# Optimization experiments

Hardware: AMD Instinct MI355X
Metric: run time of the kernel (lower is better)

Reference implementation:

```python
import jax, jax.numpy as jnp
import numpy as np

H, NH, NKV, HD, FF = 2048, 16, 8, 128, 6144
S, T = 2048, 4096
EPS, THETA, NEG = 1e-6, 1e6, -1e9

def _rms(x, w, eps=EPS):
    return x * jax.lax.rsqrt(jnp.mean(x * x, axis=-1, keepdims=True) + eps) * w

def _rotate_half(x):
    d = x.shape[-1] // 2
    return jnp.concatenate([-x[..., d:], x[..., :d]], axis=-1)

def _rope(positions, hd, theta=THETA):
    inv_freq = 1.0 / (theta ** (jnp.arange(0, hd, 2, dtype=jnp.float32) / hd))
    freqs = positions.astype(jnp.float32)[..., None] * inv_freq  # [B,S,hd/2]
    emb = jnp.concatenate([freqs, freqs], axis=-1)               # [B,S,hd]
    return jnp.cos(emb), jnp.sin(emb)

def setup_inputs() -> dict:
    key = jax.random.key(0)
    ks = jax.random.split(key, 12)
    hidden_states = jax.random.normal(ks[0], (1, S, H), jnp.float32) * 0.02
    i = jnp.arange(T)
    causal_mask = jnp.where(i[None, :] <= i[:, None], 0.0, NEG).astype(jnp.float32)[None, None]
    idxs = jnp.sort(jax.random.randint(ks[1], (S,), 0, T - 1, jnp.int32)).at[-1].set(T - 1)
    w = lambda k, sh: jax.random.normal(k, sh, jnp.float32) * 0.02
    return dict(
        hidden_states=hidden_states, causal_mask=causal_mask,
        keys_idxs=idxs, hs_idxs=idxs, positions=idxs[None, :],
        ln_in_w=jnp.ones((H,), jnp.float32),
        q_w=w(ks[2], (H, NH * HD)), k_w=w(ks[3], (H, NKV * HD)), v_w=w(ks[4], (H, NKV * HD)),
        q_norm_w=jnp.ones((HD,), jnp.float32), k_norm_w=jnp.ones((HD,), jnp.float32),
        o_w=w(ks[5], (NH * HD, H)), ln_post_w=jnp.ones((H,), jnp.float32),
        gate_w=w(ks[6], (H, FF)), up_w=w(ks[7], (H, FF)), down_w=w(ks[8], (FF, H)),
    )

def reference(hidden_states, causal_mask, keys_idxs, hs_idxs, positions,
              ln_in_w, q_w, k_w, v_w, q_norm_w, k_norm_w, o_w,
              ln_post_w, gate_w, up_w, down_w):
    B, Sq, _ = hidden_states.shape
    hd = q_norm_w.shape[0]
    nh = q_w.shape[1] // hd
    nkv = k_w.shape[1] // hd
    scaling = hd ** -0.5

    # gather pruned causal mask: index_select dim 3 (keys), then dim 2 (queries)
    mask = causal_mask[:, :, :, keys_idxs][:, :, hs_idxs, :]  # [B,1,Sq,Sk]

    cos, sin = _rope(positions, hd)  # [B,Sq,hd]

    x = _rms(hidden_states, ln_in_w)
    q = _rms((x @ q_w).reshape(B, Sq, nh, hd), q_norm_w).swapaxes(1, 2)   # [B,nh,Sq,hd]
    k = _rms((x @ k_w).reshape(B, Sq, nkv, hd), k_norm_w).swapaxes(1, 2)  # [B,nkv,Sq,hd]
    v = (x @ v_w).reshape(B, Sq, nkv, hd).swapaxes(1, 2)

    c, s = cos[:, None], sin[:, None]
    q = q * c + _rotate_half(q) * s
    k = k * c + _rotate_half(k) * s

    groups = nh // nkv
    k_rep = jnp.repeat(k, groups, axis=1)
    v_rep = jnp.repeat(v, groups, axis=1)

    # token-importance from last query (last original token kept at slot Sq-1)
    q_last = q[:, :, -1:, :]
    imp = jax.nn.softmax(jnp.einsum('bhqd,bhkd->bhqk', q_last, k_rep) * scaling, axis=-1)
    importance = imp[0, :, 0, :].mean(axis=0)
    importance = jax.lax.stop_gradient(importance.at[Sq - 1].set(jnp.inf))

    scores = jnp.einsum('bhqd,bhkd->bhqk', q, k_rep) * scaling + mask
    attn = jax.nn.softmax(scores, axis=-1)
    ctx = jnp.einsum('bhqk,bhkd->bhqd', attn, v_rep)
    attn_out = ctx.swapaxes(1, 2).reshape(B, Sq, nh * hd) @ o_w

    h = hidden_states + attn_out
    y = _rms(h, ln_post_w)
    mlp = (jax.nn.silu(y @ gate_w) * (y @ up_w)) @ down_w
    out = h + mlp
    return out, importance
```

## Files before the change

kernel.cpp:

```cpp
#include <hip/hip_runtime.h>
#include <math.h>

#define S_LEN 2048
#define HDIM  2048
#define NHEADS 16
#define NKVH   8
#define HD     128
#define FFDIM  6144
#define EPSV   1e-6f

__device__ __forceinline__ ushort f2bf(float f) {
    unsigned u = __float_as_uint(f);
    u += 0x7FFF + ((u >> 16) & 1);
    return (ushort)(u >> 16);
}
__device__ __forceinline__ float bf2f(ushort h) {
    return __uint_as_float(((unsigned)h) << 16);
}

typedef __attribute__((ext_vector_type(8))) short bf16x8;
typedef __attribute__((ext_vector_type(4))) float f32x4;

__device__ __forceinline__ void glds16(const void* g, void* l) {
    __builtin_amdgcn_global_load_lds(
        (const __attribute__((address_space(1))) void*)g,
        (__attribute__((address_space(3))) void*)l, 16, 0, 0);
}

__global__ __launch_bounds__(256) void rmsnorm_split_k(const float* __restrict__ in,
                                                       const float* __restrict__ w,
                                                       ushort* __restrict__ oh,
                                                       ushort* __restrict__ ol) {
    int s = blockIdx.x;
    int tid = threadIdx.x;
    const float* row = in + (size_t)s * HDIM;
    float ss = 0.0f;
    for (int i = tid; i < HDIM; i += 256) {
        float v = row[i];
        ss += v * v;
    }
    __shared__ float red[256];
    red[tid] = ss;
    __syncthreads();
    for (int off = 128; off > 0; off >>= 1) {
        if (tid < off) red[tid] += red[tid + off];
        __syncthreads();
    }
    float r = rsqrtf(red[0] / (float)HDIM + EPSV);
    for (int i = tid; i < HDIM; i += 256) {
        float v = row[i] * r * w[i];
        ushort h = f2bf(v);
        oh[(size_t)s * HDIM + i] = h;
        ol[(size_t)s * HDIM + i] = f2bf(v - bf2f(h));
    }
}

__global__ __launch_bounds__(256) void split_k(const float* __restrict__ in,
                                               ushort* __restrict__ oh,
                                               ushort* __restrict__ ol, int n) {
    int i = blockIdx.x * 256 + threadIdx.x;
    if (i < n) {
        float v = in[i];
        ushort h = f2bf(v);
        oh[i] = h;
        ol[i] = f2bf(v - bf2f(h));
    }
}

__global__ __launch_bounds__(256) void conv_k_swz_k(const float* __restrict__ in,
                                                    ushort* __restrict__ oh,
                                                    ushort* __restrict__ ol) {
    int i = blockIdx.x * 256 + threadIdx.x;
    int s = i >> 10;
    int d = i & 127;
    int base = i & ~127;
    float v = in[i];
    unsigned u = __float_as_uint(v);
    float hi = __uint_as_float(u & 0xFFFF0000u);
    int o = base + (d ^ ((s & 7) << 3));
    oh[o] = (ushort)(u >> 16);
    ol[o] = (ushort)(__float_as_uint(v - hi) >> 16);
}

__global__ __launch_bounds__(256) void conv_vt_k(const float* __restrict__ v,
                                                 ushort* __restrict__ oh,
                                                 ushort* __restrict__ ol) {
    __shared__ float t[64][65];
    int s0 = blockIdx.x * 64, d0 = blockIdx.y * 64, kvh = blockIdx.z;
    int tid = threadIdx.x;
#pragma unroll
    for (int p = 0; p < 4; ++p) {
        int c = tid + p * 256;
        int ss = c >> 4, d4 = (c & 15) * 4;
        float4 x = *(const float4*)&v[((size_t)(s0 + ss) * NKVH + kvh) * HD + d0 + d4];
        t[d4 + 0][ss] = x.x;
        t[d4 + 1][ss] = x.y;
        t[d4 + 2][ss] = x.z;
        t[d4 + 3][ss] = x.w;
    }
    __syncthreads();
#pragma unroll
    for (int p = 0; p < 4; ++p) {
        int c = tid + p * 256;
        int dd = c >> 4, s4 = (c & 15) * 4;
        int d = d0 + dd;
        int sx = s4 ^ ((d & 7) << 3);
        size_t obase = ((size_t)kvh * HD + d) * S_LEN + s0 + sx;
        ushort4 hv, lv;
        float a0 = t[dd][s4 + 0], a1 = t[dd][s4 + 1], a2 = t[dd][s4 + 2], a3 = t[dd][s4 + 3];
        unsigned u0 = __float_as_uint(a0), u1 = __float_as_uint(a1);
        unsigned u2 = __float_as_uint(a2), u3 = __float_as_uint(a3);
        hv.x = (ushort)(u0 >> 16); lv.x = (ushort)(__float_as_uint(a0 - __uint_as_float(u0 & 0xFFFF0000u)) >> 16);
        hv.y = (ushort)(u1 >> 16); lv.y = (ushort)(__float_as_uint(a1 - __uint_as_float(u1 & 0xFFFF0000u)) >> 16);
        hv.z = (ushort)(u2 >> 16); lv.z = (ushort)(__float_as_uint(a2 - __uint_as_float(u2 & 0xFFFF0000u)) >> 16);
        hv.w = (ushort)(u3 >> 16); lv.w = (ushort)(__float_as_uint(a3 - __uint_as_float(u3 & 0xFFFF0000u)) >> 16);
        *(ushort4*)&oh[obase] = hv;
        *(ushort4*)&ol[obase] = lv;
    }
}

__global__ __launch_bounds__(256) void transpose_split_k(const float* __restrict__ W,
                                                         ushort* __restrict__ Th,
                                                         ushort* __restrict__ Tl,
                                                         int K, int Ntot, int n0) {
    __shared__ float t[64][65];
    int tid = threadIdx.x;
    int nt = blockIdx.x * 64;
    int kt = blockIdx.y * 64;
#pragma unroll
    for (int p = 0; p < 4; ++p) {
        int idx = tid + p * 256;
        int kk = idx >> 4;
        int nn = (idx & 15) * 4;
        float4 v = *(const float4*)&W[(size_t)(kt + kk) * Ntot + n0 + nt + nn];
        t[nn + 0][kk] = v.x;
        t[nn + 1][kk] = v.y;
        t[nn + 2][kk] = v.z;
        t[nn + 3][kk] = v.w;
    }
    __syncthreads();
#pragma unroll
    for (int p = 0; p < 4; ++p) {
        int idx = tid + p * 256;
        int nn = idx >> 4;
        int kk = (idx & 15) * 4;
        ushort4 hv, lv;
        float a0 = t[nn][kk + 0], a1 = t[nn][kk + 1], a2 = t[nn][kk + 2], a3 = t[nn][kk + 3];
        hv.x = f2bf(a0); lv.x = f2bf(a0 - bf2f(hv.x));
        hv.y = f2bf(a1); lv.y = f2bf(a1 - bf2f(hv.y));
        hv.z = f2bf(a2); lv.z = f2bf(a2 - bf2f(hv.z));
        hv.w = f2bf(a3); lv.w = f2bf(a3 - bf2f(hv.w));
        size_t o = (size_t)(nt + nn) * K + kt + kk;
        *(ushort4*)&Th[o] = hv;
        *(ushort4*)&Tl[o] = lv;
    }
}

template <int MODE>
__global__ __launch_bounds__(256, 3) void gemm_bf16x3(
    const ushort* __restrict__ Ah, const ushort* __restrict__ Al,
    const ushort* __restrict__ Bh, const ushort* __restrict__ Bl,
    const float* res, const float* __restrict__ gbuf,
    float* C, ushort* __restrict__ Dh, ushort* __restrict__ Dl,
    int M, int N, int K) {
    __shared__ __align__(16) ushort sAh[128 * 32];
    __shared__ __align__(16) ushort sAl[128 * 32];
    __shared__ __align__(16) ushort sBh[128 * 32];
    __shared__ __align__(16) ushort sBl[128 * 32];

    unsigned nbx = gridDim.x;
    unsigned flat = blockIdx.y * nbx + blockIdx.x;
    unsigned cpx = (nbx * gridDim.y) >> 3;
    unsigned sflat = (flat & 7u) * cpx + (flat >> 3);
    int bx = (int)(sflat % nbx);
    int by = (int)(sflat / nbx);
    int bm = by * 128, bn = bx * 128;

    int tid = threadIdx.x;
    int lane = tid & 63, wave = tid >> 6;
    int wr = wave >> 1, wc = wave & 1;
    int r = lane & 15, kq = lane >> 4;

    int srow = tid >> 2;
    int sk = (tid & 3) * 8;
    const ushort* gA0h = Ah + (size_t)(bm + srow) * K + sk;
    const ushort* gA0l = Al + (size_t)(bm + srow) * K + sk;
    const ushort* gB0h = Bh + (size_t)(bn + srow) * K + sk;
    const ushort* gB0l = Bl + (size_t)(bn + srow) * K + sk;
    const size_t rstep = (size_t)64 * K;

    const ushort* pAh = sAh + (wr * 64 + r) * 32 + kq * 8;
    const ushort* pAl = sAl + (wr * 64 + r) * 32 + kq * 8;
    const ushort* pBh = sBh + (wc * 64 + r) * 32 + kq * 8;
    const ushort* pBl = sBl + (wc * 64 + r) * 32 + kq * 8;

    f32x4 acc[4][4] = {};

    for (int k0 = 0; k0 < K; k0 += 32) {
        glds16(gA0h, sAh + tid * 8);
        glds16(gA0h + rstep, sAh + 2048 + tid * 8);
        glds16(gA0l, sAl + tid * 8);
        glds16(gA0l + rstep, sAl + 2048 + tid * 8);
        glds16(gB0h, sBh + tid * 8);
        glds16(gB0h + rstep, sBh + 2048 + tid * 8);
        glds16(gB0l, sBl + tid * 8);
        glds16(gB0l + rstep, sBl + 2048 + tid * 8);
        gA0h += 32; gA0l += 32; gB0h += 32; gB0l += 32;
        __syncthreads();

        bf16x8 ah[4], al[4];
#pragma unroll
        for (int mi = 0; mi < 4; ++mi) {
            ah[mi] = *(const bf16x8*)(pAh + mi * 512);
            al[mi] = *(const bf16x8*)(pAl + mi * 512);
        }
#pragma unroll
        for (int ni = 0; ni < 4; ++ni) {
            bf16x8 bh = *(const bf16x8*)(pBh + ni * 512);
            bf16x8 bl = *(const bf16x8*)(pBl + ni * 512);
#pragma unroll
            for (int mi = 0; mi < 4; ++mi) {
                acc[mi][ni] = __builtin_amdgcn_mfma_f32_16x16x32_bf16(ah[mi], bh, acc[mi][ni], 0, 0, 0);
                acc[mi][ni] = __builtin_amdgcn_mfma_f32_16x16x32_bf16(al[mi], bh, acc[mi][ni], 0, 0, 0);
                acc[mi][ni] = __builtin_amdgcn_mfma_f32_16x16x32_bf16(ah[mi], bl, acc[mi][ni], 0, 0, 0);
            }
        }
        __syncthreads();
    }

    int c0 = bn + wc * 64 + r;
    int r0 = bm + wr * 64 + kq * 4;
#pragma unroll
    for (int mi = 0; mi < 4; ++mi)
#pragma unroll
        for (int ni = 0; ni < 4; ++ni)
#pragma unroll
            for (int j = 0; j < 4; ++j) {
                int row = r0 + mi * 16 + j;
                int col = c0 + ni * 16;
                size_t idx = (size_t)row * N + col;
                float val = acc[mi][ni][j];
                if (MODE == 0) {
                    if (res) val += res[idx];
                    C[idx] = val;
                } else {
                    float gv = gbuf[idx];
                    float dv = gv / (1.0f + expf(-gv)) * val;
                    ushort hh = f2bf(dv);
                    Dh[idx] = hh;
                    Dl[idx] = f2bf(dv - bf2f(hh));
                }
            }
}

__global__ __launch_bounds__(128) void qk_norm_rope_k(float* __restrict__ qk,
                                                      const float* __restrict__ nw,
                                                      const int* __restrict__ positions,
                                                      int nheads) {
    int s = blockIdx.x;
    int h = blockIdx.y;
    int d = threadIdx.x;
    float* row = qk + ((size_t)s * nheads + h) * HD;
    __shared__ float buf[HD];
    __shared__ float red[HD];
    float v = row[d];
    red[d] = v * v;
    __syncthreads();
    for (int off = 64; off > 0; off >>= 1) {
        if (d < off) red[d] += red[d + off];
        __syncthreads();
    }
    float r = rsqrtf(red[0] / (float)HD + EPSV);
    float nv = v * r * nw[d];
    buf[d] = nv;
    __syncthreads();
    float pos = (float)positions[s];
    int d2 = d & 63;
    float inv_freq = expf(-((float)(2 * d2) / 128.0f) * 13.815510557964274f);
    float freq = pos * inv_freq;
    float c, sn;
    sincosf(freq, &sn, &c);
    float rot = (d < 64) ? -buf[d + 64] : buf[d - 64];
    row[d] = nv * c + rot * sn;
}

#define ATQ 64
#define ATK 64

__global__ __launch_bounds__(256, 2) void attn_mfma_k(
    const ushort* __restrict__ Qhg, const ushort* __restrict__ Qlg,
    const ushort* __restrict__ Khg, const ushort* __restrict__ Klg,
    const ushort* __restrict__ Vhg, const ushort* __restrict__ Vlg,
    const int* __restrict__ keys_idxs, const int* __restrict__ hs_idxs,
    ushort* __restrict__ Chg, ushort* __restrict__ Clg) {
    __shared__ __align__(16) ushort sKh[64 * 128];
    __shared__ __align__(16) ushort sKl[64 * 128];
    __shared__ __align__(16) ushort sVh[128 * 64];
    __shared__ __align__(16) ushort sVl[128 * 64];
    __shared__ int kidx[ATK];
    __shared__ int qpos[ATQ];

    int bx = blockIdx.x;
    int qt = (bx & 1) ? (31 - (bx >> 1)) : (bx >> 1);
    int h = blockIdx.y;
    int kvh = h >> 1;
    int tid = threadIdx.x;
    int lane = tid & 63, wv = tid >> 6;
    int q0 = qt * ATQ;
    int r = lane & 15, kq = lane >> 4;
    int xorv = (lane & 7) << 3;
    const float scale = 0.088388347648318447f;

    bf16x8 qh[4], ql[4];
    {
        const ushort* qb = Qhg + ((size_t)(q0 + wv * 16 + r) * NHEADS + h) * HD + kq * 8;
        const ushort* qb2 = Qlg + ((size_t)(q0 + wv * 16 + r) * NHEADS + h) * HD + kq * 8;
#pragma unroll
        for (int ks = 0; ks < 4; ++ks) {
            qh[ks] = *(const bf16x8*)(qb + ks * 32);
            ql[ks] = *(const bf16x8*)(qb2 + ks * 32);
        }
    }
    if (tid < ATQ) qpos[tid] = hs_idxs[q0 + tid];

    const size_t kvstride = (size_t)NKVH * HD;
    const ushort* gKh = Khg + ((size_t)(tid >> 4) * NKVH + kvh) * HD + (tid & 15) * 8;
    const ushort* gKl = Klg + ((size_t)(tid >> 4) * NKVH + kvh) * HD + (tid & 15) * 8;
    const ushort* gVh = Vhg + ((size_t)kvh * HD + (tid >> 3)) * S_LEN + (tid & 7) * 8;
    const ushort* gVl = Vlg + ((size_t)kvh * HD + (tid >> 3)) * S_LEN + (tid & 7) * 8;

    f32x4 o[8] = {};
    float m_run[4] = {-3.0e38f, -3.0e38f, -3.0e38f, -3.0e38f};
    float l_run[4] = {0.0f, 0.0f, 0.0f, 0.0f};

    __syncthreads();
    int hs_max = qpos[ATQ - 1];
    int qp[4];
#pragma unroll
    for (int j = 0; j < 4; ++j) qp[j] = qpos[wv * 16 + kq * 4 + j];

    for (int kt = 0; kt < S_LEN / ATK; ++kt) {
        int k0 = kt * ATK;
        if (keys_idxs[k0] > hs_max) break;
        __syncthreads();
        const size_t koff = (size_t)k0 * kvstride;
#pragma unroll
        for (int p = 0; p < 4; ++p) {
            glds16(gKh + koff + (size_t)p * 16 * kvstride, sKh + (tid + p * 256) * 8);
            glds16(gKl + koff + (size_t)p * 16 * kvstride, sKl + (tid + p * 256) * 8);
            glds16(gVh + k0 + (size_t)p * 32 * S_LEN, sVh + (tid + p * 256) * 8);
            glds16(gVl + k0 + (size_t)p * 32 * S_LEN, sVl + (tid + p * 256) * 8);
        }
        if (tid < ATK) kidx[tid] = keys_idxs[k0 + tid];
        __syncthreads();

        f32x4 sf[4] = {};
#pragma unroll
        for (int ks = 0; ks < 4; ++ks) {
            int kb = (ks * 32 + kq * 8) ^ xorv;
#pragma unroll
            for (int f = 0; f < 4; ++f) {
                bf16x8 kh = *(const bf16x8*)(sKh + (f * 16 + r) * 128 + kb);
                bf16x8 kl = *(const bf16x8*)(sKl + (f * 16 + r) * 128 + kb);
                sf[f] = __builtin_amdgcn_mfma_f32_16x16x32_bf16(qh[ks], kh, sf[f], 0, 0, 0);
                sf[f] = __builtin_amdgcn_mfma_f32_16x16x32_bf16(ql[ks], kh, sf[f], 0, 0, 0);
                sf[f] = __builtin_amdgcn_mfma_f32_16x16x32_bf16(qh[ks], kl, sf[f], 0, 0, 0);
            }
        }

        int kj[4];
#pragma unroll
        for (int f = 0; f < 4; ++f) kj[f] = kidx[f * 16 + r];
        float alj[4];
#pragma unroll
        for (int j = 0; j < 4; ++j) {
#pragma unroll
            for (int f = 0; f < 4; ++f)
                sf[f][j] = sf[f][j] * scale + ((kj[f] <= qp[j]) ? 0.0f : -1.0e9f);
            float m0 = fmaxf(fmaxf(sf[0][j], sf[1][j]), fmaxf(sf[2][j], sf[3][j]));
#pragma unroll
            for (int off = 1; off < 16; off <<= 1) m0 = fmaxf(m0, __shfl_xor(m0, off));
            float mn = fmaxf(m_run[j], m0);
            alj[j] = __expf(m_run[j] - mn);
            m_run[j] = mn;
            float rsum = 0.0f;
#pragma unroll
            for (int f = 0; f < 4; ++f) {
                sf[f][j] = __expf(sf[f][j] - mn);
                rsum += sf[f][j];
            }
#pragma unroll
            for (int off = 1; off < 16; off <<= 1) rsum += __shfl_xor(rsum, off);
            l_run[j] = l_run[j] * alj[j] + rsum;
        }
#pragma unroll
        for (int df = 0; df < 8; ++df)
#pragma unroll
            for (int j = 0; j < 4; ++j) o[df][j] *= alj[j];

        __syncthreads();

        ushort* sPh = sKh + wv * 2048;
        ushort* sPl = sPh + 1024;
#pragma unroll
        for (int j = 0; j < 4; ++j) {
            int qloc = kq * 4 + j;
            int swz = (qloc & 7) << 3;
            int rowb = qloc * 64;
#pragma unroll
            for (int f = 0; f < 4; ++f) {
                float pv = sf[f][j];
                unsigned u = __float_as_uint(pv);
                float hi = __uint_as_float(u & 0xFFFF0000u);
                int a = rowb + ((f * 16 + r) ^ swz);
                sPh[a] = (ushort)(u >> 16);
                sPl[a] = (ushort)(__float_as_uint(pv - hi) >> 16);
            }
        }

#pragma unroll
        for (int kv0 = 0; kv0 < 2; ++kv0) {
            int kb = (kv0 * 32 + kq * 8) ^ xorv;
            bf16x8 pah = *(const bf16x8*)(sPh + r * 64 + kb);
            bf16x8 pal = *(const bf16x8*)(sPl + r * 64 + kb);
#pragma unroll
            for (int df = 0; df < 8; ++df) {
                bf16x8 vh = *(const bf16x8*)(sVh + (df * 16 + r) * 64 + kb);
                bf16x8 vl = *(const bf16x8*)(sVl + (df * 16 + r) * 64 + kb);
                o[df] = __builtin_amdgcn_mfma_f32_16x16x32_bf16(pah, vh, o[df], 0, 0, 0);
                o[df] = __builtin_amdgcn_mfma_f32_16x16x32_bf16(pal, vh, o[df], 0, 0, 0);
                o[df] = __builtin_amdgcn_mfma_f32_16x16x32_bf16(pah, vl, o[df], 0, 0, 0);
            }
        }
    }

#pragma unroll
    for (int j = 0; j < 4; ++j) {
        float invl = 1.0f / l_run[j];
        int qg = q0 + wv * 16 + kq * 4 + j;
#pragma unroll
        for (int df = 0; df < 8; ++df) {
            int d = df * 16 + r;
            float val = o[df][j] * invl;
            size_t idx = ((size_t)qg * NHEADS + h) * HD + d;
            ushort hh = f2bf(val);
            Chg[idx] = hh;
            Clg[idx] = f2bf(val - bf2f(hh));
        }
    }
}

__global__ __launch_bounds__(256) void importance_scores_k(const float* __restrict__ q,
                                                           const float* __restrict__ k,
                                                           float* __restrict__ imp_ws) {
    int h = blockIdx.x;
    int kv = h >> 1;
    int tid = threadIdx.x;
    __shared__ float qrow[HD];
    __shared__ float sc[S_LEN];
    __shared__ float red[256];
    const float* qp = q + ((size_t)(S_LEN - 1) * NHEADS + h) * HD;
    if (tid < HD) qrow[tid] = qp[tid];
    __syncthreads();
    const float scale = 0.088388347648318447f;
    float lmax = -3.0e38f;
#pragma unroll
    for (int rep = 0; rep < 8; ++rep) {
        int j = tid + rep * 256;
        const float* kp = k + ((size_t)j * NKVH + kv) * HD;
        float dot = 0.0f;
        for (int d = 0; d < HD; ++d) dot += qrow[d] * kp[d];
        float sval = dot * scale;
        sc[j] = sval;
        lmax = fmaxf(lmax, sval);
    }
    red[tid] = lmax;
    __syncthreads();
    for (int off = 128; off > 0; off >>= 1) {
        if (tid < off) red[tid] = fmaxf(red[tid], red[tid + off]);
        __syncthreads();
    }
    float m = red[0];
    __syncthreads();
    float lsum = 0.0f;
    float evals[8];
#pragma unroll
    for (int rep = 0; rep < 8; ++rep) {
        int j = tid + rep * 256;
        float e = expf(sc[j] - m);
        evals[rep] = e;
        lsum += e;
    }
    red[tid] = lsum;
    __syncthreads();
    for (int off = 128; off > 0; off >>= 1) {
        if (tid < off) red[tid] += red[tid + off];
        __syncthreads();
    }
    float inv = 1.0f / red[0];
#pragma unroll
    for (int rep = 0; rep < 8; ++rep) {
        int j = tid + rep * 256;
        imp_ws[(size_t)h * S_LEN + j] = evals[rep] * inv;
    }
}

__global__ __launch_bounds__(256) void importance_combine_k(const float* __restrict__ imp_ws,
                                                            float* __restrict__ out) {
    int j = blockIdx.x * 256 + threadIdx.x;
    float sum = 0.0f;
    for (int h = 0; h < NHEADS; ++h) sum += imp_ws[(size_t)h * S_LEN + j];
    out[j] = (j == S_LEN - 1) ? 3.0e38f : sum * (1.0f / NHEADS);
}

extern "C" void kernel_launch(void* const* d_in, const int* in_sizes, int n_in,
                              void* d_out, int out_size, void* d_ws, size_t ws_size,
                              hipStream_t stream) {
    const float* hidden    = (const float*)d_in[0];
    const int*   keys_idxs = (const int*)d_in[2];
    const int*   hs_idxs   = (const int*)d_in[3];
    const int*   positions = (const int*)d_in[4];
    const float* ln_in_w   = (const float*)d_in[5];
    const float* q_w       = (const float*)d_in[6];
    const float* k_w       = (const float*)d_in[7];
    const float* v_w       = (const float*)d_in[8];
    const float* q_norm_w  = (const float*)d_in[9];
    const float* k_norm_w  = (const float*)d_in[10];
    const float* o_w       = (const float*)d_in[11];
    const float* ln_post_w = (const float*)d_in[12];
    const float* gate_w    = (const float*)d_in[13];
    const float* up_w      = (const float*)d_in[14];
    const float* down_w    = (const float*)d_in[15];

    float* out = (float*)d_out;
    float* ws = (float*)d_ws;
    const size_t MF = 1024ull * 1024;

    ushort* Xh = (ushort*)(ws);
    ushort* Xl = (ushort*)(ws + 2 * MF);
    ushort* Wh = (ushort*)(ws + 4 * MF);
    ushort* Wl = (ushort*)(ws + 6 * MF);
    float*  qb  = ws + 8 * MF;
    float*  kbf = ws + 12 * MF;
    float*  vbf = ws + 14 * MF;
    ushort* Qbh = (ushort*)(ws);
    ushort* Qbl = (ushort*)(ws + 2 * MF);
    float*  imp = ws + 4 * MF;
    ushort* Kbh = (ushort*)(ws + 4 * MF);
    ushort* Kbl = (ushort*)(ws + 5 * MF);
    ushort* Vth = (ushort*)(ws + 6 * MF);
    ushort* Vtl = (ushort*)(ws + 7 * MF);
    ushort* Ch = (ushort*)(ws + 8 * MF);
    ushort* Cl = (ushort*)(ws + 10 * MF);
    float*  hb = ws + 12 * MF;
    ushort* Yh = (ushort*)(ws + 16 * MF);
    ushort* Yl = (ushort*)(ws + 18 * MF);
    float*  gb = ws + 8 * MF;
    ushort* Dh = (ushort*)(ws + 12 * MF);
    ushort* Dl = (ushort*)(ws + 14 * MF);

    rmsnorm_split_k<<<S_LEN, 256, 0, stream>>>(hidden, ln_in_w, Xh, Xl);

    transpose_split_k<<<dim3(32, 32), 256, 0, stream>>>(q_w, Wh, Wl, HDIM, HDIM, 0);
    gemm_bf16x3<0><<<dim3(HDIM / 128, S_LEN / 128), 256, 0, stream>>>(
        Xh, Xl, Wh, Wl, nullptr, nullptr, qb, nullptr, nullptr, S_LEN, HDIM, HDIM);

    transpose_split_k<<<dim3(16, 32), 256, 0, stream>>>(k_w, Wh, Wl, HDIM, 1024, 0);
    gemm_bf16x3<0><<<dim3(1024 / 128, S_LEN / 128), 256, 0, stream>>>(
        Xh, Xl, Wh, Wl, nullptr, nullptr, kbf, nullptr, nullptr, S_LEN, 1024, HDIM);

    transpose_split_k<<<dim3(16, 32), 256, 0, stream>>>(v_w, Wh, Wl, HDIM, 1024, 0);
    gemm_bf16x3<0><<<dim3(1024 / 128, S_LEN / 128), 256, 0, stream>>>(
        Xh, Xl, Wh, Wl, nullptr, nullptr, vbf, nullptr, nullptr, S_LEN, 1024, HDIM);

    qk_norm_rope_k<<<dim3(S_LEN, NHEADS), 128, 0, stream>>>(qb, q_norm_w, positions, NHEADS);
    qk_norm_rope_k<<<dim3(S_LEN, NKVH), 128, 0, stream>>>(kbf, k_norm_w, positions, NKVH);

    importance_scores_k<<<NHEADS, 256, 0, stream>>>(qb, kbf, imp);
    importance_combine_k<<<S_LEN / 256, 256, 0, stream>>>(imp, out + (size_t)S_LEN * HDIM);

    split_k<<<(S_LEN * NHEADS * HD) / 256, 256, 0, stream>>>(qb, Qbh, Qbl, S_LEN * NHEADS * HD);
    conv_k_swz_k<<<(S_LEN * NKVH * HD) / 256, 256, 0, stream>>>(kbf, Kbh, Kbl);
    conv_vt_k<<<dim3(S_LEN / 64, HD / 64, NKVH), 256, 0, stream>>>(vbf, Vth, Vtl);

    attn_mfma_k<<<dim3(S_LEN / ATQ, NHEADS), 256, 0, stream>>>(
        Qbh, Qbl, Kbh, Kbl, Vth, Vtl, keys_idxs, hs_idxs, Ch, Cl);

    transpose_split_k<<<dim3(32, 32), 256, 0, stream>>>(o_w, Wh, Wl, HDIM, HDIM, 0);
    gemm_bf16x3<0><<<dim3(HDIM / 128, S_LEN / 128), 256, 0, stream>>>(
        Ch, Cl, Wh, Wl, hidden, nullptr, hb, nullptr, nullptr, S_LEN, HDIM, HDIM);

    hipMemcpyAsync(out, hb, (size_t)S_LEN * HDIM * sizeof(float),
                   hipMemcpyDeviceToDevice, stream);

    rmsnorm_split_k<<<S_LEN, 256, 0, stream>>>(hb, ln_post_w, Yh, Yl);

    for (int c = 0; c < 3; ++c) {
        transpose_split_k<<<dim3(32, 32), 256, 0, stream>>>(gate_w, Wh, Wl, HDIM, FFDIM, c * 2048);
        gemm_bf16x3<0><<<dim3(16, 16), 256, 0, stream>>>(
            Yh, Yl, Wh, Wl, nullptr, nullptr, gb, nullptr, nullptr, S_LEN, 2048, HDIM);
        transpose_split_k<<<dim3(32, 32), 256, 0, stream>>>(up_w, Wh, Wl, HDIM, FFDIM, c * 2048);
        gemm_bf16x3<1><<<dim3(16, 16), 256, 0, stream>>>(
            Yh, Yl, Wh, Wl, nullptr, gb, nullptr, Dh, Dl, S_LEN, 2048, HDIM);
        transpose_split_k<<<dim3(32, 32), 256, 0, stream>>>(
            down_w + (size_t)c * 2048 * HDIM, Wh, Wl, 2048, HDIM, 0);
        gemm_bf16x3<0><<<dim3(16, 16), 256, 0, stream>>>(
            Dh, Dl, Wh, Wl, out, nullptr, out, nullptr, nullptr, S_LEN, HDIM, 2048);
    }
}
```

Baseline: 1.687 ms.

## Double-buffer GEMM LDS staging and merge QKV and gate/up GEMMs

The GEMM kernel now double-buffers its LDS tiles, so the global-to-LDS load of the next K slice is issued before the MFMA work on the current one, and one barrier per iteration is removed. Occupancy drops to 2 blocks per CU because LDS use doubles. The Q/K/V projections are merged into one wide GEMM writing a strided qkv buffer, and gate/up are merged into one N=4096 GEMM. SiLU*mul moves into a separate elementwise kernel, which adds an extra round trip through global memory but gives larger launches and reuses the A tiles.

```diff
diff --git a/kernel.cpp b/kernel.cpp
--- a/kernel.cpp
+++ b/kernel.cpp
@@ -55,34 +55,32 @@
     }
 }
 
-__global__ __launch_bounds__(256) void split_k(const float* __restrict__ in,
-                                               ushort* __restrict__ oh,
-                                               ushort* __restrict__ ol, int n) {
+__global__ __launch_bounds__(256) void conv_q_k(const float* __restrict__ in,
+                                                ushort* __restrict__ oh,
+                                                ushort* __restrict__ ol) {
     int i = blockIdx.x * 256 + threadIdx.x;
-    if (i < n) {
-        float v = in[i];
-        ushort h = f2bf(v);
-        oh[i] = h;
-        ol[i] = f2bf(v - bf2f(h));
-    }
+    int s = i >> 11, c = i & 2047;
+    float v = in[(size_t)s * 4096 + c];
+    ushort h = f2bf(v);
+    oh[i] = h;
+    ol[i] = f2bf(v - bf2f(h));
 }
 
 __global__ __launch_bounds__(256) void conv_k_swz_k(const float* __restrict__ in,
                                                     ushort* __restrict__ oh,
                                                     ushort* __restrict__ ol) {
     int i = blockIdx.x * 256 + threadIdx.x;
-    int s = i >> 10;
-    int d = i & 127;
-    int base = i & ~127;
-    float v = in[i];
+    int s = i >> 10, c = i & 1023;
+    int d = c & 127;
+    float v = in[(size_t)s * 4096 + 2048 + c];
     unsigned u = __float_as_uint(v);
     float hi = __uint_as_float(u & 0xFFFF0000u);
-    int o = base + (d ^ ((s & 7) << 3));
+    int o = (i & ~127) + (d ^ ((s & 7) << 3));
     oh[o] = (ushort)(u >> 16);
     ol[o] = (ushort)(__float_as_uint(v - hi) >> 16);
 }
 
-__global__ __launch_bounds__(256) void conv_vt_k(const float* __restrict__ v,
+__global__ __launch_bounds__(256) void conv_vt_k(const float* __restrict__ vsrc,
                                                  ushort* __restrict__ oh,
                                                  ushort* __restrict__ ol) {
     __shared__ float t[64][65];
@@ -92,7 +90,7 @@
     for (int p = 0; p < 4; ++p) {
         int c = tid + p * 256;
         int ss = c >> 4, d4 = (c & 15) * 4;
-        float4 x = *(const float4*)&v[((size_t)(s0 + ss) * NKVH + kvh) * HD + d0 + d4];
+        float4 x = *(const float4*)&vsrc[(size_t)(s0 + ss) * 4096 + 3072 + kvh * 128 + d0 + d4];
         t[d4 + 0][ss] = x.x;
         t[d4 + 1][ss] = x.y;
         t[d4 + 2][ss] = x.z;
@@ -122,7 +120,8 @@
 __global__ __launch_bounds__(256) void transpose_split_k(const float* __restrict__ W,
                                                          ushort* __restrict__ Th,
                                                          ushort* __restrict__ Tl,
-                                                         int K, int Ntot, int n0) {
+                                                         int K, int Ntot, int n0,
+                                                         int nout0) {
     __shared__ float t[64][65];
     int tid = threadIdx.x;
     int nt = blockIdx.x * 64;
@@ -150,23 +149,21 @@
         hv.y = f2bf(a1); lv.y = f2bf(a1 - bf2f(hv.y));
         hv.z = f2bf(a2); lv.z = f2bf(a2 - bf2f(hv.z));
         hv.w = f2bf(a3); lv.w = f2bf(a3 - bf2f(hv.w));
-        size_t o = (size_t)(nt + nn) * K + kt + kk;
+        size_t o = (size_t)(nout0 + nt + nn) * K + kt + kk;
         *(ushort4*)&Th[o] = hv;
         *(ushort4*)&Tl[o] = lv;
     }
 }
 
-template <int MODE>
-__global__ __launch_bounds__(256, 3) void gemm_bf16x3(
+__global__ __launch_bounds__(256, 2) void gemm_bf16x3(
     const ushort* __restrict__ Ah, const ushort* __restrict__ Al,
     const ushort* __restrict__ Bh, const ushort* __restrict__ Bl,
-    const float* res, const float* __restrict__ gbuf,
-    float* C, ushort* __restrict__ Dh, ushort* __restrict__ Dl,
+    const float* __restrict__ res, float* __restrict__ C,
     int M, int N, int K) {
-    __shared__ __align__(16) ushort sAh[128 * 32];
-    __shared__ __align__(16) ushort sAl[128 * 32];
-    __shared__ __align__(16) ushort sBh[128 * 32];
-    __shared__ __align__(16) ushort sBl[128 * 32];
+    __shared__ __align__(16) ushort sAh[2][128 * 32];
+    __shared__ __align__(16) ushort sAl[2][128 * 32];
+    __shared__ __align__(16) ushort sBh[2][128 * 32];
+    __shared__ __align__(16) ushort sBl[2][128 * 32];
 
     unsigned nbx = gridDim.x;
     unsigned flat = blockIdx.y * nbx + blockIdx.x;
@@ -183,31 +180,29 @@
 
     int srow = tid >> 2;
     int sk = (tid & 3) * 8;
-    const ushort* gA0h = Ah + (size_t)(bm + srow) * K + sk;
-    const ushort* gA0l = Al + (size_t)(bm + srow) * K + sk;
-    const ushort* gB0h = Bh + (size_t)(bn + srow) * K + sk;
-    const ushort* gB0l = Bl + (size_t)(bn + srow) * K + sk;
+    const ushort* gAh = Ah + (size_t)(bm + srow) * K + sk;
+    const ushort* gAl = Al + (size_t)(bm + srow) * K + sk;
+    const ushort* gBh = Bh + (size_t)(bn + srow) * K + sk;
+    const ushort* gBl = Bl + (size_t)(bn + srow) * K + sk;
     const size_t rstep = (size_t)64 * K;
 
-    const ushort* pAh = sAh + (wr * 64 + r) * 32 + kq * 8;
-    const ushort* pAl = sAl + (wr * 64 + r) * 32 + kq * 8;
-    const ushort* pBh = sBh + (wc * 64 + r) * 32 + kq * 8;
-    const ushort* pBl = sBl + (wc * 64 + r) * 32 + kq * 8;
-
     f32x4 acc[4][4] = {};
 
-    for (int k0 = 0; k0 < K; k0 += 32) {
-        glds16(gA0h, sAh + tid * 8);
-        glds16(gA0h + rstep, sAh + 2048 + tid * 8);
-        glds16(gA0l, sAl + tid * 8);
-        glds16(gA0l + rstep, sAl + 2048 + tid * 8);
-        glds16(gB0h, sBh + tid * 8);
-        glds16(gB0h + rstep, sBh + 2048 + tid * 8);
-        glds16(gB0l, sBl + tid * 8);
-        glds16(gB0l + rstep, sBl + 2048 + tid * 8);
-        gA0h += 32; gA0l += 32; gB0h += 32; gB0l += 32;
-        __syncthreads();
-
+    auto STAGE = [&](int buf, int k0) {
+        glds16(gAh + k0, &sAh[buf][tid * 8]);
+        glds16(gAh + k0 + rstep, &sAh[buf][2048 + tid * 8]);
+        glds16(gAl + k0, &sAl[buf][tid * 8]);
+        glds16(gAl + k0 + rstep, &sAl[buf][2048 + tid * 8]);
+        glds16(gBh + k0, &sBh[buf][tid * 8]);
+        glds16(gBh + k0 + rstep, &sBh[buf][2048 + tid * 8]);
+        glds16(gBl + k0, &sBl[buf][tid * 8]);
+        glds16(gBl + k0 + rstep, &sBl[buf][2048 + tid * 8]);
+    };
+    auto COMPUTE = [&](int buf) {
+        const ushort* pAh = &sAh[buf][(wr * 64 + r) * 32 + kq * 8];
+        const ushort* pAl = &sAl[buf][(wr * 64 + r) * 32 + kq * 8];
+        const ushort* pBh = &sBh[buf][(wc * 64 + r) * 32 + kq * 8];
+        const ushort* pBl = &sBl[buf][(wc * 64 + r) * 32 + kq * 8];
         bf16x8 ah[4], al[4];
 #pragma unroll
         for (int mi = 0; mi < 4; ++mi) {
@@ -225,8 +220,18 @@
                 acc[mi][ni] = __builtin_amdgcn_mfma_f32_16x16x32_bf16(ah[mi], bl, acc[mi][ni], 0, 0, 0);
             }
         }
-        __syncthreads();
-    }
+    };
+
+    STAGE(0, 0);
+    __syncthreads();
+    int cur = 0;
+    for (int k0 = 32; k0 < K; k0 += 32) {
+        STAGE(cur ^ 1, k0);
+        COMPUTE(cur);
+        __syncthreads();
+        cur ^= 1;
+    }
+    COMPUTE(cur);
 
     int c0 = bn + wc * 64 + r;
     int r0 = bm + wr * 64 + kq * 4;
@@ -240,27 +245,19 @@
                 int col = c0 + ni * 16;
                 size_t idx = (size_t)row * N + col;
                 float val = acc[mi][ni][j];
-                if (MODE == 0) {
-                    if (res) val += res[idx];
-                    C[idx] = val;
-                } else {
-                    float gv = gbuf[idx];
-                    float dv = gv / (1.0f + expf(-gv)) * val;
-                    ushort hh = f2bf(dv);
-                    Dh[idx] = hh;
-                    Dl[idx] = f2bf(dv - bf2f(hh));
-                }
+                if (res) val += res[idx];
+                C[idx] = val;
             }
 }
 
 __global__ __launch_bounds__(128) void qk_norm_rope_k(float* __restrict__ qk,
                                                       const float* __restrict__ nw,
                                                       const int* __restrict__ positions,
-                                                      int nheads) {
+                                                      int stride) {
     int s = blockIdx.x;
     int h = blockIdx.y;
     int d = threadIdx.x;
-    float* row = qk + ((size_t)s * nheads + h) * HD;
+    float* row = qk + (size_t)s * stride + (size_t)h * HD;
     __shared__ float buf[HD];
     __shared__ float red[HD];
     float v = row[d];
@@ -452,14 +449,15 @@
 
 __global__ __launch_bounds__(256) void importance_scores_k(const float* __restrict__ q,
                                                            const float* __restrict__ k,
-                                                           float* __restrict__ imp_ws) {
+                                                           float* __restrict__ imp_ws,
+                                                           int stride) {
     int h = blockIdx.x;
     int kv = h >> 1;
     int tid = threadIdx.x;
     __shared__ float qrow[HD];
     __shared__ float sc[S_LEN];
     __shared__ float red[256];
-    const float* qp = q + ((size_t)(S_LEN - 1) * NHEADS + h) * HD;
+    const float* qp = q + (size_t)(S_LEN - 1) * stride + (size_t)h * HD;
     if (tid < HD) qrow[tid] = qp[tid];
     __syncthreads();
     const float scale = 0.088388347648318447f;
@@ -467,7 +465,7 @@
 #pragma unroll
     for (int rep = 0; rep < 8; ++rep) {
         int j = tid + rep * 256;
-        const float* kp = k + ((size_t)j * NKVH + kv) * HD;
+        const float* kp = k + (size_t)j * stride + (size_t)kv * HD;
         float dot = 0.0f;
         for (int d = 0; d < HD; ++d) dot += qrow[d] * kp[d];
         float sval = dot * scale;
@@ -511,6 +509,19 @@
     float sum = 0.0f;
     for (int h = 0; h < NHEADS; ++h) sum += imp_ws[(size_t)h * S_LEN + j];
     out[j] = (j == S_LEN - 1) ? 3.0e38f : sum * (1.0f / NHEADS);
+}
+
+__global__ __launch_bounds__(256) void silu_split_k(const float* __restrict__ gu,
+                                                    ushort* __restrict__ dh,
+                                                    ushort* __restrict__ dl) {
+    int i = blockIdx.x * 256 + threadIdx.x;
+    int s = i >> 11, c = i & 2047;
+    const float* row = gu + (size_t)s * 4096;
+    float g = row[c], u = row[c + 2048];
+    float d = g / (1.0f + expf(-g)) * u;
+    ushort hh = f2bf(d);
+    dh[i] = hh;
+    dl[i] = f2bf(d - bf2f(hh));
 }
 
 extern "C" void kernel_launch(void* const* d_in, const int* in_sizes, int n_in,
@@ -536,59 +547,55 @@
     float* ws = (float*)d_ws;
     const size_t MF = 1024ull * 1024;
 
-    ushort* Xh = (ushort*)(ws);
-    ushort* Xl = (ushort*)(ws + 2 * MF);
-    ushort* Wh = (ushort*)(ws + 4 * MF);
-    ushort* Wl = (ushort*)(ws + 6 * MF);
-    float*  qb  = ws + 8 * MF;
-    float*  kbf = ws + 12 * MF;
-    float*  vbf = ws + 14 * MF;
+    ushort* Xh  = (ushort*)(ws);
+    ushort* Xl  = (ushort*)(ws + 2 * MF);
+    ushort* Wh  = (ushort*)(ws + 4 * MF);
+    ushort* Wl  = (ushort*)(ws + 8 * MF);
+    float*  qkv = ws + 12 * MF;
     ushort* Qbh = (ushort*)(ws);
     ushort* Qbl = (ushort*)(ws + 2 * MF);
-    float*  imp = ws + 4 * MF;
     ushort* Kbh = (ushort*)(ws + 4 * MF);
     ushort* Kbl = (ushort*)(ws + 5 * MF);
     ushort* Vth = (ushort*)(ws + 6 * MF);
     ushort* Vtl = (ushort*)(ws + 7 * MF);
-    ushort* Ch = (ushort*)(ws + 8 * MF);
-    ushort* Cl = (ushort*)(ws + 10 * MF);
-    float*  hb = ws + 12 * MF;
-    ushort* Yh = (ushort*)(ws + 16 * MF);
-    ushort* Yl = (ushort*)(ws + 18 * MF);
-    float*  gb = ws + 8 * MF;
-    ushort* Dh = (ushort*)(ws + 12 * MF);
-    ushort* Dl = (ushort*)(ws + 14 * MF);
+    float*  imp = ws + 8 * MF;
+    ushort* Woh = (ushort*)(ws + 4 * MF);
+    ushort* Wol = (ushort*)(ws + 6 * MF);
+    ushort* Ch  = (ushort*)(ws + 12 * MF);
+    ushort* Cl  = (ushort*)(ws + 14 * MF);
+    float*  hb  = ws + 16 * MF;
+    ushort* Yh  = (ushort*)(ws);
+    ushort* Yl  = (ushort*)(ws + 2 * MF);
+    float*  gu  = ws + 12 * MF;
+    ushort* Dh  = (ushort*)(ws + 4 * MF);
+    ushort* Dl  = (ushort*)(ws + 6 * MF);
+    ushort* Wdh = (ushort*)(ws + 8 * MF);
+    ushort* Wdl = (ushort*)(ws + 10 * MF);
 
     rmsnorm_split_k<<<S_LEN, 256, 0, stream>>>(hidden, ln_in_w, Xh, Xl);
 
-    transpose_split_k<<<dim3(32, 32), 256, 0, stream>>>(q_w, Wh, Wl, HDIM, HDIM, 0);
-    gemm_bf16x3<0><<<dim3(HDIM / 128, S_LEN / 128), 256, 0, stream>>>(
-        Xh, Xl, Wh, Wl, nullptr, nullptr, qb, nullptr, nullptr, S_LEN, HDIM, HDIM);
-
-    transpose_split_k<<<dim3(16, 32), 256, 0, stream>>>(k_w, Wh, Wl, HDIM, 1024, 0);
-    gemm_bf16x3<0><<<dim3(1024 / 128, S_LEN / 128), 256, 0, stream>>>(
-        Xh, Xl, Wh, Wl, nullptr, nullptr, kbf, nullptr, nullptr, S_LEN, 1024, HDIM);
-
-    transpose_split_k<<<dim3(16, 32), 256, 0, stream>>>(v_w, Wh, Wl, HDIM, 1024, 0);
-    gemm_bf16x3<0><<<dim3(1024 / 128, S_LEN / 128), 256, 0, stream>>>(
-        Xh, Xl, Wh, Wl, nullptr, nullptr, vbf, nullptr, nullptr, S_LEN, 1024, HDIM);
-
-    qk_norm_rope_k<<<dim3(S_LEN, NHEADS), 128, 0, stream>>>(qb, q_norm_w, positions, NHEADS);
-    qk_norm_rope_k<<<dim3(S_LEN, NKVH), 128, 0, stream>>>(kbf, k_norm_w, positions, NKVH);
-
-    importance_scores_k<<<NHEADS, 256, 0, stream>>>(qb, kbf, imp);
+    transpose_split_k<<<dim3(32, 32), 256, 0, stream>>>(q_w, Wh, Wl, HDIM, HDIM, 0, 0);
+    transpose_split_k<<<dim3(16, 32), 256, 0, stream>>>(k_w, Wh, Wl, HDIM, 1024, 0, 2048);
+    transpose_split_k<<<dim3(16, 32), 256, 0, stream>>>(v_w, Wh, Wl, HDIM, 1024, 0, 3072);
+    gemm_bf16x3<<<dim3(4096 / 128, S_LEN / 128), 256, 0, stream>>>(
+        Xh, Xl, Wh, Wl, nullptr, qkv, S_LEN, 4096, HDIM);
+
+    qk_norm_rope_k<<<dim3(S_LEN, NHEADS), 128, 0, stream>>>(qkv, q_norm_w, positions, 4096);
+    qk_norm_rope_k<<<dim3(S_LEN, NKVH), 128, 0, stream>>>(qkv + 2048, k_norm_w, positions, 4096);
+
+    importance_scores_k<<<NHEADS, 256, 0, stream>>>(qkv, qkv + 2048, imp, 4096);
     importance_combine_k<<<S_LEN / 256, 256, 0, stream>>>(imp, out + (size_t)S_LEN * HDIM);
 
-    split_k<<<(S_LEN * NHEADS * HD) / 256, 256, 0, stream>>>(qb, Qbh, Qbl, S_LEN * NHEADS * HD);
-    conv_k_swz_k<<<(S_LEN * NKVH * HD) / 256, 256, 0, stream>>>(kbf, Kbh, Kbl);
-    conv_vt_k<<<dim3(S_LEN / 64, HD / 64, NKVH), 256, 0, stream>>>(vbf, Vth, Vtl);
+    conv_q_k<<<(S_LEN * 2048) / 256, 256, 0, stream>>>(qkv, Qbh, Qbl);
+    conv_k_swz_k<<<(S_LEN * 1024) / 256, 256, 0, stream>>>(qkv, Kbh, Kbl);
+    conv_vt_k<<<dim3(S_LEN / 64, HD / 64, NKVH), 256, 0, stream>>>(qkv, Vth, Vtl);
 
     attn_mfma_k<<<dim3(S_LEN / ATQ, NHEADS), 256, 0, stream>>>(
         Qbh, Qbl, Kbh, Kbl, Vth, Vtl, keys_idxs, hs_idxs, Ch, Cl);
 
-    transpose_split_k<<<dim3(32, 32), 256, 0, stream>>>(o_w, Wh, Wl, HDIM, HDIM, 0);
-    gemm_bf16x3<0><<<dim3(HDIM / 128, S_LEN / 128), 256, 0, stream>>>(
-        Ch, Cl, Wh, Wl, hidden, nullptr, hb, nullptr, nullptr, S_LEN, HDIM, HDIM);
+    transpose_split_k<<<dim3(32, 32), 256, 0, stream>>>(o_w, Woh, Wol, HDIM, HDIM, 0, 0);
+    gemm_bf16x3<<<dim3(HDIM / 128, S_LEN / 128), 256, 0, stream>>>(
+        Ch, Cl, Woh, Wol, hidden, hb, S_LEN, HDIM, HDIM);
 
     hipMemcpyAsync(out, hb, (size_t)S_LEN * HDIM * sizeof(float),
                    hipMemcpyDeviceToDevice, stream);
@@ -596,15 +603,14 @@
     rmsnorm_split_k<<<S_LEN, 256, 0, stream>>>(hb, ln_post_w, Yh, Yl);
 
     for (int c = 0; c < 3; ++c) {
-        transpose_split_k<<<dim3(32, 32), 256, 0, stream>>>(gate_w, Wh, Wl, HDIM, FFDIM, c * 2048);
-        gemm_bf16x3<0><<<dim3(16, 16), 256, 0, stream>>>(
-            Yh, Yl, Wh, Wl, nullptr, nullptr, gb, nullptr, nullptr, S_LEN, 2048, HDIM);
-        transpose_split_k<<<dim3(32, 32), 256, 0, stream>>>(up_w, Wh, Wl, HDIM, FFDIM, c * 2048);
-        gemm_bf16x3<1><<<dim3(16, 16), 256, 0, stream>>>(
-            Yh, Yl, Wh, Wl, nullptr, gb, nullptr, Dh, Dl, S_LEN, 2048, HDIM);
+        transpose_split_k<<<dim3(32, 32), 256, 0, stream>>>(gate_w, Wh, Wl, HDIM, FFDIM, c * 2048, 0);
+        transpose_split_k<<<dim3(32, 32), 256, 0, stream>>>(up_w, Wh, Wl, HDIM, FFDIM, c * 2048, 2048);
+        gemm_bf16x3<<<dim3(4096 / 128, S_LEN / 128), 256, 0, stream>>>(
+            Yh, Yl, Wh, Wl, nullptr, gu, S_LEN, 4096, HDIM);
+        silu_split_k<<<(S_LEN * 2048) / 256, 256, 0, stream>>>(gu, Dh, Dl);
         transpose_split_k<<<dim3(32, 32), 256, 0, stream>>>(
-            down_w + (size_t)c * 2048 * HDIM, Wh, Wl, 2048, HDIM, 0);
-        gemm_bf16x3<0><<<dim3(16, 16), 256, 0, stream>>>(
-            Dh, Dl, Wh, Wl, out, nullptr, out, nullptr, nullptr, S_LEN, HDIM, 2048);
-    }
-}
+            down_w + (size_t)c * 2048 * HDIM, Wdh, Wdl, 2048, HDIM, 0, 0);
+        gemm_bf16x3<<<dim3(HDIM / 128, S_LEN / 128), 256, 0, stream>>>(
+            Dh, Dl, Wdh, Wdl, out, out, S_LEN, HDIM, 2048);
+    }
+}
```

Result: faster. 1.362 ms (-19.3%).
